# Kernel tuning notes

Hardware: AMD Instinct MI355X
Metric: run time of the kernel (lower is better)

Reference implementation:

```python
import jax, jax.numpy as jnp
import numpy as np

# CSSA config (index=0): H=W=64, strip windows h_spa=64, w_spa=8, heads=4, C=64
B, HW, C, HEADS = 32, 64, 64, 4
HS, WS = 64, 8          # h_spa, w_spa
HD = C // HEADS          # head_dim = 16
WIN = HS * WS            # 512 tokens per window
SCALE = HD ** -0.5


def setup_inputs() -> dict:
    key = jax.random.key(0)
    k1, k2, k3 = jax.random.split(key, 3)
    qkv = jax.random.normal(k1, (3, B, HW * HW, C), dtype=jnp.float32)
    w_conv = jax.random.normal(k2, (C, 1, 3, 3), dtype=jnp.float32) * 0.1
    b_conv = jax.random.normal(k3, (C,), dtype=jnp.float32) * 0.1
    return {"qkv": qkv, "w_conv": w_conv, "b_conv": b_conv}


def _to_img(x):
    # [B, N, C] -> [B, C, H, W]
    return jnp.transpose(x.reshape(B, HW, HW, C), (0, 3, 1, 2))


def _img2window_heads(x):
    img = _to_img(x)
    img = img.reshape(B, C, HW // HS, HS, HW // WS, WS)
    win = jnp.transpose(img, (0, 2, 4, 3, 5, 1)).reshape(-1, WIN, C)
    return jnp.transpose(win.reshape(-1, WIN, HEADS, HD), (0, 2, 1, 3))


def _v_windows(x):
    # [B, N, C] -> [B*nWin, C, h_spa, w_spa] (image-layout windows for conv)
    img = _to_img(x)
    img = img.reshape(B, C, HW // HS, HS, HW // WS, WS)
    return jnp.transpose(img, (0, 2, 4, 1, 3, 5)).reshape(-1, C, HS, WS)


def reference(qkv, w_conv, b_conv):
    q, k, v = qkv[0], qkv[1], qkv[2]
    qh = _img2window_heads(q) * SCALE
    kh = _img2window_heads(k)
    vw = _v_windows(v)                           # [Bw, C, HS, WS]
    # depthwise 3x3 conv LePE
    lepe = jax.lax.conv_general_dilated(
        vw, w_conv, window_strides=(1, 1), padding=((1, 1), (1, 1)),
        feature_group_count=C,
        dimension_numbers=("NCHW", "OIHW", "NCHW")) + b_conv[None, :, None, None]
    Bw = vw.shape[0]
    lepe = jnp.transpose(lepe.reshape(Bw, HEADS, HD, WIN), (0, 1, 3, 2))
    vh = jnp.transpose(vw.reshape(Bw, HEADS, HD, WIN), (0, 1, 3, 2))
    attn = jax.nn.softmax(jnp.einsum("whqd,whkd->whqk", qh, kh), axis=-1)
    x = jnp.einsum("whqk,whkd->whqd", attn, vh) + lepe
    x = jnp.transpose(x, (0, 2, 1, 3)).reshape(Bw, WIN, C)
    # window2spa
    x = x.reshape(B, HW // HS, HW // WS, HS, WS, C)
    x = jnp.transpose(x, (0, 1, 3, 2, 4, 5)).reshape(B, HW * HW, C)
    return x
```

## Files before the change

kernel.cpp:

```cpp
#include <hip/hip_runtime.h>
#include <stdint.h>

#define KSTR2 20
#define VSTR  520

typedef __attribute__((ext_vector_type(4))) short          short4v;
typedef __attribute__((ext_vector_type(8))) short          short8v;
typedef __attribute__((ext_vector_type(4))) float          f32x4;
typedef __attribute__((ext_vector_type(4))) unsigned short us4;

#define HAVE_MFMA16 __has_builtin(__builtin_amdgcn_mfma_f32_16x16x16bf16_1k)

__device__ __forceinline__ float bf2f(unsigned short u) {
    union { unsigned int i; float f; } x; x.i = ((unsigned int)u) << 16; return x.f;
}
__device__ __forceinline__ unsigned short f2bf(float f) {
    union { float f; unsigned int u; } x; x.f = f;
    return (unsigned short)((x.u + 0x8000u) >> 16);
}
__device__ __forceinline__ unsigned int pk2bf(float lo, float hi) {
    union { float f; unsigned int u; } a, b; a.f = lo; b.f = hi;
    return __builtin_amdgcn_perm(b.u + 0x8000u, a.u + 0x8000u, 0x07060302u);
}

__global__ __launch_bounds__(256, 4)
void CSSA_69355131896243_kernel(const float* __restrict__ qkv,
                                const float* __restrict__ wconv,
                                const float* __restrict__ bconv,
                                float* __restrict__ out)
{
    __shared__ unsigned short Kl[512 * KSTR2];
    __shared__ unsigned short Vt[16 * VSTR];
    __shared__ float Wl[144];
    __shared__ float Bl[16];

    const int tid  = threadIdx.x;
    const int wave = tid >> 6, lane = tid & 63, quad = lane >> 4, l15 = lane & 15;

    const int bid = blockIdx.x;
    const int win = (bid & 7) * 32 + ((bid >> 3) >> 2);
    const int h   = (bid >> 3) & 3;
    const int b   = win >> 3, wx = win & 7;

    const size_t ONE  = (size_t)32 * 4096 * 64;
    const size_t base = ((size_t)b * 4096 + (size_t)wx * 8) * 64;
    const float* gQ = qkv + base;
    const float* gK = qkv + ONE + base;
    const float* gV = qkv + 2 * ONE + base;

    if (tid < 144) Wl[tid] = wconv[h * 144 + tid];
    if (tid < 16)  Bl[tid] = bconv[h * 16 + tid];

    {
        const int t4 = tid >> 2;
        const int c4 = tid & 3;
        for (int r = 0; r < 8; ++r) {
            const int t = r * 64 + t4;
            const size_t goff = (size_t)(t >> 3) * 4096 + (size_t)(t & 7) * 64 + h * 16 + c4 * 4;
            f32x4 kd = *(const f32x4*)(gK + goff);
            f32x4 vd = *(const f32x4*)(gV + goff);
            us4 kb;
            #pragma unroll
            for (int j = 0; j < 4; ++j) kb[j] = f2bf(kd[j]);
            *(us4*)(&Kl[t * KSTR2 + c4 * 4]) = kb;
            #pragma unroll
            for (int j = 0; j < 4; ++j) Vt[(c4 * 4 + j) * VSTR + t] = f2bf(vd[j]);
        }
    }

    const float SCL = 0.25f * 1.44269504088896341f;
#if HAVE_MFMA16
    f32x4 qv[8];
    #pragma unroll
    for (int t = 0; t < 8; ++t) {
        const int q = wave * 128 + t * 16 + l15;
        qv[t] = *(const f32x4*)(gQ + (size_t)(q >> 3) * 4096 + (size_t)(q & 7) * 64 + h * 16 + quad * 4);
    }
#else
    f32x4 qv0[8], qv1[8];
    #pragma unroll
    for (int t = 0; t < 8; ++t) {
        const int q = wave * 128 + t * 16 + l15;
        const size_t off = (size_t)(q >> 3) * 4096 + (size_t)(q & 7) * 64 + h * 16 + (quad & 1) * 8;
        qv0[t] = *(const f32x4*)(gQ + off);
        qv1[t] = *(const f32x4*)(gQ + off + 4);
    }
#endif
    __syncthreads();

#if HAVE_MFMA16
    short4v qf[8];
    #pragma unroll
    for (int t = 0; t < 8; ++t) {
        union { short4v s; unsigned int u[2]; } p;
        p.u[0] = pk2bf(qv[t][0] * SCL, qv[t][1] * SCL);
        p.u[1] = pk2bf(qv[t][2] * SCL, qv[t][3] * SCL);
        qf[t] = p.s;
    }
#else
    short8v qf[8];
    #pragma unroll
    for (int t = 0; t < 8; ++t) {
        short8v f = (short8v)0;
        if (quad < 2) {
            union { short4v s; unsigned int u[2]; } pa, pb;
            pa.u[0] = pk2bf(qv0[t][0] * SCL, qv0[t][1] * SCL);
            pa.u[1] = pk2bf(qv0[t][2] * SCL, qv0[t][3] * SCL);
            pb.u[0] = pk2bf(qv1[t][0] * SCL, qv1[t][1] * SCL);
            pb.u[1] = pk2bf(qv1[t][2] * SCL, qv1[t][3] * SCL);
            #pragma unroll
            for (int i = 0; i < 4; ++i) { f[i] = pa.s[i]; f[4 + i] = pb.s[i]; }
        }
        qf[t] = f;
    }
#endif

    f32x4 acc[8];
    float lp[8];
    #pragma unroll
    for (int t = 0; t < 8; ++t) { acc[t] = (f32x4)0.0f; lp[t] = 0.0f; }

#if HAVE_MFMA16
    short4v kf = *(const short4v*)(&Kl[l15 * KSTR2 + quad * 4]);
    short4v vf = *(const short4v*)(&Vt[l15 * VSTR + quad * 4]);
    for (int c = 0; c < 32; ++c) {
        const int kn = ((c + 1) & 31) * 16;
        short4v kf_n = *(const short4v*)(&Kl[(kn + l15) * KSTR2 + quad * 4]);
        short4v vf_n = *(const short4v*)(&Vt[l15 * VSTR + kn + quad * 4]);
        #pragma unroll
        for (int t = 0; t < 8; ++t) {
            f32x4 s = __builtin_amdgcn_mfma_f32_16x16x16bf16_1k(kf, qf[t], (f32x4)0.0f, 0, 0, 0);
            float p0 = __builtin_amdgcn_exp2f(s[0]);
            float p1 = __builtin_amdgcn_exp2f(s[1]);
            float p2 = __builtin_amdgcn_exp2f(s[2]);
            float p3 = __builtin_amdgcn_exp2f(s[3]);
            lp[t] += (p0 + p1) + (p2 + p3);
            union { short4v s4; unsigned int u[2]; } pf;
            pf.u[0] = pk2bf(p0, p1);
            pf.u[1] = pk2bf(p2, p3);
            acc[t] = __builtin_amdgcn_mfma_f32_16x16x16bf16_1k(vf, pf.s4, acc[t], 0, 0, 0);
        }
        kf = kf_n; vf = vf_n;
    }
#else
    const int bidx0 = (((quad & 1) * 2) * 16 + l15) * 4;
    const int bidx1 = bidx0 + 64;
    for (int c = 0; c < 16; ++c) {
        const int k0 = c * 32;
        short8v kfA = (short8v)0, kfB = (short8v)0;
        if (quad < 2) {
            const short4v a0 = *(const short4v*)(&Kl[(k0 + l15) * KSTR2 + quad * 8]);
            const short4v a1 = *(const short4v*)(&Kl[(k0 + l15) * KSTR2 + quad * 8 + 4]);
            const short4v b0 = *(const short4v*)(&Kl[(k0 + 16 + l15) * KSTR2 + quad * 8]);
            const short4v b1 = *(const short4v*)(&Kl[(k0 + 16 + l15) * KSTR2 + quad * 8 + 4]);
            #pragma unroll
            for (int i = 0; i < 4; ++i) { kfA[i] = a0[i]; kfA[4 + i] = a1[i]; kfB[i] = b0[i]; kfB[4 + i] = b1[i]; }
        }
        const short8v vf8 = *(const short8v*)(&Vt[l15 * VSTR + k0 + quad * 8]);
        #pragma unroll
        for (int t = 0; t < 8; ++t) {
            f32x4 s0 = __builtin_amdgcn_mfma_f32_16x16x32_bf16(kfA, qf[t], (f32x4)0.0f, 0, 0, 0);
            f32x4 s1 = __builtin_amdgcn_mfma_f32_16x16x32_bf16(kfB, qf[t], (f32x4)0.0f, 0, 0, 0);
            float e0[4], e1[4];
            #pragma unroll
            for (int j = 0; j < 4; ++j) {
                e0[j] = __builtin_amdgcn_exp2f(s0[j]);
                e1[j] = __builtin_amdgcn_exp2f(s1[j]);
                lp[t] += e0[j] + e1[j];
            }
            const unsigned int a0 = pk2bf(e0[0], e0[1]), a1 = pk2bf(e0[2], e0[3]);
            const unsigned int b0 = pk2bf(e1[0], e1[1]), b1 = pk2bf(e1[2], e1[3]);
            const unsigned int s0u = (quad < 2) ? a0 : b0;
            const unsigned int s1u = (quad < 2) ? a1 : b1;
            union { short8v s8; unsigned int u[4]; } pf;
            pf.u[0] = (unsigned int)__builtin_amdgcn_ds_bpermute(bidx0, (int)s0u);
            pf.u[1] = (unsigned int)__builtin_amdgcn_ds_bpermute(bidx0, (int)s1u);
            pf.u[2] = (unsigned int)__builtin_amdgcn_ds_bpermute(bidx1, (int)s0u);
            pf.u[3] = (unsigned int)__builtin_amdgcn_ds_bpermute(bidx1, (int)s1u);
            acc[t] = __builtin_amdgcn_mfma_f32_16x16x32_bf16(vf8, pf.s8, acc[t], 0, 0, 0);
        }
    }
#endif

    float linv[8];
    #pragma unroll
    for (int t = 0; t < 8; ++t) {
        float v = lp[t];
        v += __shfl_xor(v, 16, 64);
        v += __shfl_xor(v, 32, 64);
        linv[t] = __builtin_amdgcn_rcpf(v);
    }

    #pragma unroll
    for (int j = 0; j < 4; ++j) {
        const int d = quad * 4 + j;
        float w9[9];
        #pragma unroll
        for (int o = 0; o < 9; ++o) w9[o] = Wl[d * 9 + o];
        const float bs = Bl[d];
        #pragma unroll
        for (int t = 0; t < 8; ++t) {
            const int q = wave * 128 + t * 16 + l15;
            const int y = q >> 3, x = q & 7;
            float lep = bs;
            #pragma unroll
            for (int dy = 0; dy < 3; ++dy) {
                #pragma unroll
                for (int dx = 0; dx < 3; ++dx) {
                    const int yy = y + dy - 1, xx = x + dx - 1;
                    const bool ok = ((unsigned)yy < 64u) && ((unsigned)xx < 8u);
                    const int tt = (q + (dy - 1) * 8 + (dx - 1)) & 511;
                    lep += (ok ? w9[dy * 3 + dx] : 0.0f) * bf2f(Vt[d * VSTR + tt]);
                }
            }
            acc[t][j] = acc[t][j] * linv[t] + lep;
        }
    }
    float* gO = out + base;
    #pragma unroll
    for (int t = 0; t < 8; ++t) {
        const int q = wave * 128 + t * 16 + l15;
        *(f32x4*)(gO + (size_t)(q >> 3) * 4096 + (size_t)(q & 7) * 64 + h * 16 + quad * 4) = acc[t];
    }
}

extern "C" void kernel_launch(void* const* d_in, const int* in_sizes, int n_in,
                              void* d_out, int out_size, void* d_ws, size_t ws_size,
                              hipStream_t stream) {
    const float* qkv   = (const float*)d_in[0];
    const float* wconv = (const float*)d_in[1];
    const float* bconv = (const float*)d_in[2];
    float* outp = (float*)d_out;
    hipLaunchKernelGGL(CSSA_69355131896243_kernel, dim3(1024), dim3(256), 0, stream,
                       qkv, wconv, bconv, outp);
}
```

Baseline: 202.3 us.

## Use 1024-thread blocks covering all heads and stream K from global

Each block now handles all four heads for half of a window's queries with 16 waves, loading V for every channel into LDS as a full 64-row transposed tile with coalesced 64-channel reads. K is no longer staged in LDS; each wave reads its K fragments directly from global memory with one-step register prefetch and converts them to bf16 in registers. Each wave handles 64 queries instead of 128, which lowers register pressure, and the grid halves to 512 blocks. The trade-off is that each wave reads K from global (L2) in a strided pattern, V is loaded twice per window (once per query half), and LDS use per block is larger.

```diff
diff --git a/kernel.cpp b/kernel.cpp
--- a/kernel.cpp
+++ b/kernel.cpp
@@ -1,46 +1,47 @@
 #include <hip/hip_runtime.h>
 #include <stdint.h>
 
-#define KSTR2 20
-#define VSTR  520
+#define VSTR 520
 
 typedef __attribute__((ext_vector_type(4))) short          short4v;
-typedef __attribute__((ext_vector_type(8))) short          short8v;
 typedef __attribute__((ext_vector_type(4))) float          f32x4;
-typedef __attribute__((ext_vector_type(4))) unsigned short us4;
 
-#define HAVE_MFMA16 __has_builtin(__builtin_amdgcn_mfma_f32_16x16x16bf16_1k)
-
-__device__ __forceinline__ float bf2f(unsigned short u) {
-    union { unsigned int i; float f; } x; x.i = ((unsigned int)u) << 16; return x.f;
-}
 __device__ __forceinline__ unsigned short f2bf(float f) {
     union { float f; unsigned int u; } x; x.f = f;
     return (unsigned short)((x.u + 0x8000u) >> 16);
+}
+__device__ __forceinline__ float bf2f(unsigned short u) {
+    union { unsigned int i; float f; } x; x.i = ((unsigned int)u) << 16; return x.f;
 }
 __device__ __forceinline__ unsigned int pk2bf(float lo, float hi) {
     union { float f; unsigned int u; } a, b; a.f = lo; b.f = hi;
     return __builtin_amdgcn_perm(b.u + 0x8000u, a.u + 0x8000u, 0x07060302u);
 }
+__device__ __forceinline__ short4v pk4bf(float a, float b, float c, float d) {
+    union { short4v s; unsigned int u[2]; } p;
+    p.u[0] = pk2bf(a, b);
+    p.u[1] = pk2bf(c, d);
+    return p.s;
+}
 
-__global__ __launch_bounds__(256, 4)
+__global__ __launch_bounds__(1024, 8)
 void CSSA_69355131896243_kernel(const float* __restrict__ qkv,
                                 const float* __restrict__ wconv,
                                 const float* __restrict__ bconv,
                                 float* __restrict__ out)
 {
-    __shared__ unsigned short Kl[512 * KSTR2];
-    __shared__ unsigned short Vt[16 * VSTR];
-    __shared__ float Wl[144];
-    __shared__ float Bl[16];
+    __shared__ unsigned short Vt[64 * VSTR];
+    __shared__ float Wl[576];
+    __shared__ float Bl[64];
 
     const int tid  = threadIdx.x;
     const int wave = tid >> 6, lane = tid & 63, quad = lane >> 4, l15 = lane & 15;
 
-    const int bid = blockIdx.x;
-    const int win = (bid & 7) * 32 + ((bid >> 3) >> 2);
-    const int h   = (bid >> 3) & 3;
-    const int b   = win >> 3, wx = win & 7;
+    const int bid  = blockIdx.x;
+    const int rest = bid >> 3;
+    const int qh   = rest & 1;
+    const int win  = (bid & 7) * 32 + (rest >> 1);
+    const int b    = win >> 3, wx = win & 7;
 
     const size_t ONE  = (size_t)32 * 4096 * 64;
     const size_t base = ((size_t)b * 4096 + (size_t)wx * 8) * 64;
@@ -48,143 +49,71 @@
     const float* gK = qkv + ONE + base;
     const float* gV = qkv + 2 * ONE + base;
 
-    if (tid < 144) Wl[tid] = wconv[h * 144 + tid];
-    if (tid < 16)  Bl[tid] = bconv[h * 16 + tid];
-
     {
-        const int t4 = tid >> 2;
-        const int c4 = tid & 3;
+        const int tb = tid >> 4;
+        const int c4 = (tid & 15) * 4;
+        #pragma unroll
         for (int r = 0; r < 8; ++r) {
-            const int t = r * 64 + t4;
-            const size_t goff = (size_t)(t >> 3) * 4096 + (size_t)(t & 7) * 64 + h * 16 + c4 * 4;
-            f32x4 kd = *(const f32x4*)(gK + goff);
-            f32x4 vd = *(const f32x4*)(gV + goff);
-            us4 kb;
+            const int t = r * 64 + tb;
+            f32x4 vd = *(const f32x4*)(gV + (size_t)(t >> 3) * 4096 + (size_t)(t & 7) * 64 + c4);
             #pragma unroll
-            for (int j = 0; j < 4; ++j) kb[j] = f2bf(kd[j]);
-            *(us4*)(&Kl[t * KSTR2 + c4 * 4]) = kb;
-            #pragma unroll
-            for (int j = 0; j < 4; ++j) Vt[(c4 * 4 + j) * VSTR + t] = f2bf(vd[j]);
+            for (int j = 0; j < 4; ++j) Vt[(c4 + j) * VSTR + t] = f2bf(vd[j]);
         }
     }
+    if (tid < 576) Wl[tid] = wconv[tid];
+    if (tid < 64)  Bl[tid] = bconv[tid];
+
+    const int h  = wave >> 2;
+    const int q0 = qh * 256 + (wave & 3) * 64;
+    const int hc = h * 16;
 
     const float SCL = 0.25f * 1.44269504088896341f;
-#if HAVE_MFMA16
-    f32x4 qv[8];
+    f32x4 qv[4];
     #pragma unroll
-    for (int t = 0; t < 8; ++t) {
-        const int q = wave * 128 + t * 16 + l15;
-        qv[t] = *(const f32x4*)(gQ + (size_t)(q >> 3) * 4096 + (size_t)(q & 7) * 64 + h * 16 + quad * 4);
+    for (int t = 0; t < 4; ++t) {
+        const int q = q0 + t * 16 + l15;
+        qv[t] = *(const f32x4*)(gQ + (size_t)(q >> 3) * 4096 + (size_t)(q & 7) * 64 + hc + quad * 4);
     }
-#else
-    f32x4 qv0[8], qv1[8];
-    #pragma unroll
-    for (int t = 0; t < 8; ++t) {
-        const int q = wave * 128 + t * 16 + l15;
-        const size_t off = (size_t)(q >> 3) * 4096 + (size_t)(q & 7) * 64 + h * 16 + (quad & 1) * 8;
-        qv0[t] = *(const f32x4*)(gQ + off);
-        qv1[t] = *(const f32x4*)(gQ + off + 4);
-    }
-#endif
     __syncthreads();
 
-#if HAVE_MFMA16
-    short4v qf[8];
+    short4v qf[4];
     #pragma unroll
-    for (int t = 0; t < 8; ++t) {
-        union { short4v s; unsigned int u[2]; } p;
-        p.u[0] = pk2bf(qv[t][0] * SCL, qv[t][1] * SCL);
-        p.u[1] = pk2bf(qv[t][2] * SCL, qv[t][3] * SCL);
-        qf[t] = p.s;
+    for (int t = 0; t < 4; ++t)
+        qf[t] = pk4bf(qv[t][0] * SCL, qv[t][1] * SCL, qv[t][2] * SCL, qv[t][3] * SCL);
+
+    f32x4 acc[4];
+    float lp[4];
+    #pragma unroll
+    for (int t = 0; t < 4; ++t) { acc[t] = (f32x4)0.0f; lp[t] = 0.0f; }
+
+    const float* gKh = gK + hc + quad * 4;
+    const int kt0 = l15;
+    f32x4 kv = *(const f32x4*)(gKh + (size_t)(kt0 >> 3) * 4096 + (size_t)(kt0 & 7) * 64);
+    #pragma unroll 4
+    for (int c = 0; c < 32; ++c) {
+        f32x4 kvn;
+        if (c < 31) {
+            const int t = (c + 1) * 16 + l15;
+            kvn = *(const f32x4*)(gKh + (size_t)(t >> 3) * 4096 + (size_t)(t & 7) * 64);
+        }
+        const short4v kf = pk4bf(kv[0], kv[1], kv[2], kv[3]);
+        const short4v vf = *(const short4v*)(&Vt[(hc + l15) * VSTR + c * 16 + quad * 4]);
+        #pragma unroll
+        for (int t = 0; t < 4; ++t) {
+            f32x4 s = __builtin_amdgcn_mfma_f32_16x16x16bf16_1k(kf, qf[t], (f32x4)0.0f, 0, 0, 0);
+            const float p0 = __builtin_amdgcn_exp2f(s[0]);
+            const float p1 = __builtin_amdgcn_exp2f(s[1]);
+            const float p2 = __builtin_amdgcn_exp2f(s[2]);
+            const float p3 = __builtin_amdgcn_exp2f(s[3]);
+            lp[t] += (p0 + p1) + (p2 + p3);
+            acc[t] = __builtin_amdgcn_mfma_f32_16x16x16bf16_1k(vf, pk4bf(p0, p1, p2, p3), acc[t], 0, 0, 0);
+        }
+        kv = kvn;
     }
-#else
-    short8v qf[8];
+
+    float linv[4];
     #pragma unroll
-    for (int t = 0; t < 8; ++t) {
-        short8v f = (short8v)0;
-        if (quad < 2) {
-            union { short4v s; unsigned int u[2]; } pa, pb;
-            pa.u[0] = pk2bf(qv0[t][0] * SCL, qv0[t][1] * SCL);
-            pa.u[1] = pk2bf(qv0[t][2] * SCL, qv0[t][3] * SCL);
-            pb.u[0] = pk2bf(qv1[t][0] * SCL, qv1[t][1] * SCL);
-            pb.u[1] = pk2bf(qv1[t][2] * SCL, qv1[t][3] * SCL);
-            #pragma unroll
-            for (int i = 0; i < 4; ++i) { f[i] = pa.s[i]; f[4 + i] = pb.s[i]; }
-        }
-        qf[t] = f;
-    }
-#endif
-
-    f32x4 acc[8];
-    float lp[8];
-    #pragma unroll
-    for (int t = 0; t < 8; ++t) { acc[t] = (f32x4)0.0f; lp[t] = 0.0f; }
-
-#if HAVE_MFMA16
-    short4v kf = *(const short4v*)(&Kl[l15 * KSTR2 + quad * 4]);
-    short4v vf = *(const short4v*)(&Vt[l15 * VSTR + quad * 4]);
-    for (int c = 0; c < 32; ++c) {
-        const int kn = ((c + 1) & 31) * 16;
-        short4v kf_n = *(const short4v*)(&Kl[(kn + l15) * KSTR2 + quad * 4]);
-        short4v vf_n = *(const short4v*)(&Vt[l15 * VSTR + kn + quad * 4]);
-        #pragma unroll
-        for (int t = 0; t < 8; ++t) {
-            f32x4 s = __builtin_amdgcn_mfma_f32_16x16x16bf16_1k(kf, qf[t], (f32x4)0.0f, 0, 0, 0);
-            float p0 = __builtin_amdgcn_exp2f(s[0]);
-            float p1 = __builtin_amdgcn_exp2f(s[1]);
-            float p2 = __builtin_amdgcn_exp2f(s[2]);
-            float p3 = __builtin_amdgcn_exp2f(s[3]);
-            lp[t] += (p0 + p1) + (p2 + p3);
-            union { short4v s4; unsigned int u[2]; } pf;
-            pf.u[0] = pk2bf(p0, p1);
-            pf.u[1] = pk2bf(p2, p3);
-            acc[t] = __builtin_amdgcn_mfma_f32_16x16x16bf16_1k(vf, pf.s4, acc[t], 0, 0, 0);
-        }
-        kf = kf_n; vf = vf_n;
-    }
-#else
-    const int bidx0 = (((quad & 1) * 2) * 16 + l15) * 4;
-    const int bidx1 = bidx0 + 64;
-    for (int c = 0; c < 16; ++c) {
-        const int k0 = c * 32;
-        short8v kfA = (short8v)0, kfB = (short8v)0;
-        if (quad < 2) {
-            const short4v a0 = *(const short4v*)(&Kl[(k0 + l15) * KSTR2 + quad * 8]);
-            const short4v a1 = *(const short4v*)(&Kl[(k0 + l15) * KSTR2 + quad * 8 + 4]);
-            const short4v b0 = *(const short4v*)(&Kl[(k0 + 16 + l15) * KSTR2 + quad * 8]);
-            const short4v b1 = *(const short4v*)(&Kl[(k0 + 16 + l15) * KSTR2 + quad * 8 + 4]);
-            #pragma unroll
-            for (int i = 0; i < 4; ++i) { kfA[i] = a0[i]; kfA[4 + i] = a1[i]; kfB[i] = b0[i]; kfB[4 + i] = b1[i]; }
-        }
-        const short8v vf8 = *(const short8v*)(&Vt[l15 * VSTR + k0 + quad * 8]);
-        #pragma unroll
-        for (int t = 0; t < 8; ++t) {
-            f32x4 s0 = __builtin_amdgcn_mfma_f32_16x16x32_bf16(kfA, qf[t], (f32x4)0.0f, 0, 0, 0);
-            f32x4 s1 = __builtin_amdgcn_mfma_f32_16x16x32_bf16(kfB, qf[t], (f32x4)0.0f, 0, 0, 0);
-            float e0[4], e1[4];
-            #pragma unroll
-            for (int j = 0; j < 4; ++j) {
-                e0[j] = __builtin_amdgcn_exp2f(s0[j]);
-                e1[j] = __builtin_amdgcn_exp2f(s1[j]);
-                lp[t] += e0[j] + e1[j];
-            }
-            const unsigned int a0 = pk2bf(e0[0], e0[1]), a1 = pk2bf(e0[2], e0[3]);
-            const unsigned int b0 = pk2bf(e1[0], e1[1]), b1 = pk2bf(e1[2], e1[3]);
-            const unsigned int s0u = (quad < 2) ? a0 : b0;
-            const unsigned int s1u = (quad < 2) ? a1 : b1;
-            union { short8v s8; unsigned int u[4]; } pf;
-            pf.u[0] = (unsigned int)__builtin_amdgcn_ds_bpermute(bidx0, (int)s0u);
-            pf.u[1] = (unsigned int)__builtin_amdgcn_ds_bpermute(bidx0, (int)s1u);
-            pf.u[2] = (unsigned int)__builtin_amdgcn_ds_bpermute(bidx1, (int)s0u);
-            pf.u[3] = (unsigned int)__builtin_amdgcn_ds_bpermute(bidx1, (int)s1u);
-            acc[t] = __builtin_amdgcn_mfma_f32_16x16x32_bf16(vf8, pf.s8, acc[t], 0, 0, 0);
-        }
-    }
-#endif
-
-    float linv[8];
-    #pragma unroll
-    for (int t = 0; t < 8; ++t) {
+    for (int t = 0; t < 4; ++t) {
         float v = lp[t];
         v += __shfl_xor(v, 16, 64);
         v += __shfl_xor(v, 32, 64);
@@ -194,13 +123,14 @@
     #pragma unroll
     for (int j = 0; j < 4; ++j) {
         const int d = quad * 4 + j;
+        const int ch = hc + d;
         float w9[9];
         #pragma unroll
-        for (int o = 0; o < 9; ++o) w9[o] = Wl[d * 9 + o];
-        const float bs = Bl[d];
+        for (int o = 0; o < 9; ++o) w9[o] = Wl[ch * 9 + o];
+        const float bs = Bl[ch];
         #pragma unroll
-        for (int t = 0; t < 8; ++t) {
-            const int q = wave * 128 + t * 16 + l15;
+        for (int t = 0; t < 4; ++t) {
+            const int q = q0 + t * 16 + l15;
             const int y = q >> 3, x = q & 7;
             float lep = bs;
             #pragma unroll
@@ -210,7 +140,7 @@
                     const int yy = y + dy - 1, xx = x + dx - 1;
                     const bool ok = ((unsigned)yy < 64u) && ((unsigned)xx < 8u);
                     const int tt = (q + (dy - 1) * 8 + (dx - 1)) & 511;
-                    lep += (ok ? w9[dy * 3 + dx] : 0.0f) * bf2f(Vt[d * VSTR + tt]);
+                    lep += (ok ? w9[dy * 3 + dx] : 0.0f) * bf2f(Vt[ch * VSTR + tt]);
                 }
             }
             acc[t][j] = acc[t][j] * linv[t] + lep;
@@ -218,9 +148,9 @@
     }
     float* gO = out + base;
     #pragma unroll
-    for (int t = 0; t < 8; ++t) {
-        const int q = wave * 128 + t * 16 + l15;
-        *(f32x4*)(gO + (size_t)(q >> 3) * 4096 + (size_t)(q & 7) * 64 + h * 16 + quad * 4) = acc[t];
+    for (int t = 0; t < 4; ++t) {
+        const int q = q0 + t * 16 + l15;
+        *(f32x4*)(gO + (size_t)(q >> 3) * 4096 + (size_t)(q & 7) * 64 + hc + quad * 4) = acc[t];
     }
 }
 
@@ -231,6 +161,6 @@
     const float* wconv = (const float*)d_in[1];
     const float* bconv = (const float*)d_in[2];
     float* outp = (float*)d_out;
-    hipLaunchKernelGGL(CSSA_69355131896243_kernel, dim3(1024), dim3(256), 0, stream,
+    hipLaunchKernelGGL(CSSA_69355131896243_kernel, dim3(512), dim3(1024), 0, stream,
                        qkv, wconv, bconv, outp);
 }
```

Result: slower. 499.7 us (+147.1%).
